# Kernel optimization log

Hardware: AMD Instinct MI355X
Metric: run time of the kernel (lower is better)

The kernel has to match this reference:

```python
import jax, jax.numpy as jnp
import numpy as np

L, B, S, D, H, FF = 6, 32, 512, 512, 8, 2048
DK = D // H
EPS = 1e-5
GELU_C = 0.7978845608028654  # sqrt(2/pi)
INV_SQRT_DK = 1.0 / float(np.sqrt(DK))


def gelu(x):
    return 0.5 * x * (1.0 + jnp.tanh(GELU_C * (x + 0.044715 * x ** 3)))


def layernorm(x, gamma, beta):
    m = jnp.mean(x, axis=-1, keepdims=True)
    v = jnp.mean(jnp.square(x - m), axis=-1, keepdims=True)
    return gamma * (x - m) / jnp.sqrt(v + EPS) + beta


def attention(x, WQ, WK, WV, WO):
    # NOTE: the original splits columns as (d_key, n_heads) on input,
    # and merges as (n_heads * d_key) on output -- replicated faithfully.
    q = (x @ WQ).reshape(B, S, DK, H).transpose(0, 3, 1, 2)  # (B,H,S,DK)
    k = (x @ WK).reshape(B, S, DK, H).transpose(0, 3, 2, 1)  # (B,H,DK,S)
    v = (x @ WV).reshape(B, S, DK, H).transpose(0, 3, 1, 2)  # (B,H,S,DK)
    score = jax.nn.softmax(jnp.matmul(q, k) * INV_SQRT_DK, axis=-1)  # (B,H,S,S)
    o = jnp.matmul(score, v).transpose(0, 2, 1, 3).reshape(B, S, H * DK)
    return o @ WO


def setup_inputs() -> dict:
    key = jax.random.key(0)
    ks = jax.random.split(key, 8)
    sc = 0.02
    return {
        "x": jax.random.normal(ks[0], (B, S, D), jnp.float32),
        "WQ": jax.random.normal(ks[1], (L, D, D), jnp.float32) * sc,
        "WK": jax.random.normal(ks[2], (L, D, D), jnp.float32) * sc,
        "WV": jax.random.normal(ks[3], (L, D, D), jnp.float32) * sc,
        "WO": jax.random.normal(ks[4], (L, D, D), jnp.float32) * sc,
        "K1": jax.random.normal(ks[5], (L, D, FF), jnp.float32) * sc,
        "B1": jnp.zeros((L, FF), jnp.float32),
        "K2": jax.random.normal(ks[6], (L, FF, D), jnp.float32) * sc,
        "B2": jnp.zeros((L, D), jnp.float32),
        "G1": jnp.ones((L, D), jnp.float32),
        "BE1": jnp.zeros((L, D), jnp.float32),
        "G2": jnp.ones((L, D), jnp.float32),
        "BE2": jnp.zeros((L, D), jnp.float32),
    }


def reference(x, WQ, WK, WV, WO, K1, B1, K2, B2, G1, BE1, G2, BE2):
    def step(h, p):
        wq, wk, wv, wo, k1, b1, k2, b2, g1, be1, g2, be2 = p
        h = layernorm(h + attention(h, wq, wk, wv, wo), g1, be1)
        f = gelu(h @ k1 + b1) @ k2 + b2
        h = layernorm(h + f, g2, be2)
        return h, None

    out, _ = jax.lax.scan(step, x, (WQ, WK, WV, WO, K1, B1, K2, B2, G1, BE1, G2, BE2))
    return out
```

## Files before the change

### kernel.cpp

```cpp
#include <hip/hip_runtime.h>
#include <hip/hip_bf16.h>
#include <stdint.h>

#define LB 6
#define BB 32
#define SS 512
#define DD 512
#define HH 8
#define FF_ 2048
#define MM (BB*SS)

typedef unsigned short u16;
typedef __attribute__((ext_vector_type(8))) short bf16x8;
typedef __attribute__((ext_vector_type(4))) float f32x4;

#define MFMA16(a,b,c) __builtin_amdgcn_mfma_f32_16x16x32_bf16((a),(b),(c),0,0,0)
#define GLD16(g, l) __builtin_amdgcn_global_load_lds( \
    (const __attribute__((address_space(1))) unsigned int*)(g), \
    (__attribute__((address_space(3))) unsigned int*)(l), 16, 0, 0)

__device__ __forceinline__ u16 f2b(float f){
  unsigned int u = __float_as_uint(f);
  u = u + 0x7FFFu + ((u >> 16) & 1u);
  return (u16)(u >> 16);
}

__device__ __forceinline__ float gelu_f(float x){
  float u = 0.7978845608028654f * (x + 0.044715f * x * x * x);
  return 0.5f * x * (1.0f + tanhf(u));
}

__global__ __launch_bounds__(256) void k_prep(const float* __restrict__ x,
                                              float* __restrict__ h,
                                              u16* __restrict__ hb){
  int i = blockIdx.x * 256 + threadIdx.x;
  float4 v = ((const float4*)x)[i];
  ((float4*)h)[i] = v;
  uint2 p;
  p.x = (unsigned)f2b(v.x) | ((unsigned)f2b(v.y) << 16);
  p.y = (unsigned)f2b(v.z) | ((unsigned)f2b(v.w) << 16);
  ((uint2*)hb)[i] = p;
}

__global__ __launch_bounds__(256) void k_wt(const float* __restrict__ in,
                                            u16* __restrict__ out, int K, int N){
  size_t ms = (size_t)K * N;
  in  += ms * blockIdx.z;
  out += ms * blockIdx.z;
  int n0 = blockIdx.x * 64, k0 = blockIdx.y * 64;
  __shared__ float tile[64][65];
  int t = threadIdx.x;
  int c = t & 63, rb = t >> 6;
  #pragma unroll
  for (int p = 0; p < 16; p++){
    int k = p * 4 + rb;
    tile[k][c] = in[(size_t)(k0 + k) * N + (n0 + c)];
  }
  __syncthreads();
  #pragma unroll
  for (int p = 0; p < 16; p++){
    int n = p * 4 + rb;
    out[(size_t)(n0 + n) * K + (k0 + c)] = f2b(tile[c][n]);
  }
}

template<int EPI, bool PERM>
__device__ __forceinline__ void gemm_body(const u16* __restrict__ A, const u16* __restrict__ Bt,
    const float* __restrict__ bias, float* __restrict__ outF, u16* __restrict__ outH,
    int N, int K)
{
  __shared__ u16 sA[128*32];
  __shared__ u16 sB[128*32];
  const int t = threadIdx.x;
  const int w = t >> 6, lane = t & 63, lr = lane & 15, lh = lane >> 4;
  const int bm = blockIdx.x * 128, bn = blockIdx.y * 128;
  const int wr = (w >> 1) * 64, wc = (w & 1) * 64;

  f32x4 acc[4][4];
  #pragma unroll
  for (int i = 0; i < 4; i++)
    #pragma unroll
    for (int j = 0; j < 4; j++) acc[i][j] = (f32x4){0.f,0.f,0.f,0.f};

  const int srow = t >> 2;
  const int scol = (t & 3) * 8;
  int b0 = bn + srow, b1 = bn + srow + 64;
  if (PERM){
    b0 = ((b0 & 63) << 3) | (b0 >> 6);
    b1 = ((b1 & 63) << 3) | (b1 >> 6);
  }
  const u16* gA0 = A  + (size_t)(bm + srow) * K + scol;
  const u16* gA1 = gA0 + (size_t)64 * K;
  const u16* gB0 = Bt + (size_t)b0 * K + scol;
  const u16* gB1 = Bt + (size_t)b1 * K + scol;
  u16* lA = sA + w * 512;
  u16* lB = sB + w * 512;

  for (int k0 = 0; k0 < K; k0 += 32){
    GLD16(gA0 + k0, lA);
    GLD16(gA1 + k0, lA + 2048);
    GLD16(gB0 + k0, lB);
    GLD16(gB1 + k0, lB + 2048);
    __syncthreads();
    bf16x8 af[4], bfr[4];
    #pragma unroll
    for (int i = 0; i < 4; i++) af[i]  = *(const bf16x8*)&sA[(wr + i*16 + lr)*32 + lh*8];
    #pragma unroll
    for (int j = 0; j < 4; j++) bfr[j] = *(const bf16x8*)&sB[(wc + j*16 + lr)*32 + lh*8];
    #pragma unroll
    for (int i = 0; i < 4; i++)
      #pragma unroll
      for (int j = 0; j < 4; j++)
        acc[i][j] = MFMA16(af[i], bfr[j], acc[i][j]);
    __syncthreads();
  }

  #pragma unroll
  for (int i = 0; i < 4; i++){
    int row = bm + wr + i*16 + lh*4;
    #pragma unroll
    for (int j = 0; j < 4; j++){
      int col = bn + wc + j*16 + lr;
      float bv = (EPI >= 2) ? bias[col] : 0.f;
      #pragma unroll
      for (int r = 0; r < 4; r++){
        float v = acc[i][j][r];
        size_t o = (size_t)(row + r) * N + col;
        if (EPI == 0) outH[o] = f2b(v);
        else if (EPI == 1) outF[o] = v;
        else if (EPI == 2) outH[o] = f2b(gelu_f(v + bv));
        else outF[o] = v + bv;
      }
    }
  }
}

template<int EPI>
__global__ __launch_bounds__(256) void k_gemm(const u16* A, const u16* Bt, const float* bias,
                                              float* outF, u16* outH, int N, int K){
  gemm_body<EPI,false>(A, Bt, bias, outF, outH, N, K);
}

__global__ __launch_bounds__(256) void k_qkv(const u16* A, const u16* Bq, const u16* Bk, const u16* Bv,
                                             u16* oq, u16* ok, u16* ov){
  const u16* Bt = (blockIdx.z == 0) ? Bq : (blockIdx.z == 1) ? Bk : Bv;
  u16* out = (blockIdx.z == 0) ? oq : (blockIdx.z == 1) ? ok : ov;
  gemm_body<0,true>(A, Bt, nullptr, nullptr, out, DD, DD);
}

__global__ __launch_bounds__(256) void k_attn(const u16* __restrict__ Q, const u16* __restrict__ Kp,
                                              const u16* __restrict__ V, u16* __restrict__ O){
  const int qt = blockIdx.x, hh = blockIdx.y, b = blockIdx.z;
  __shared__ u16 Qs[64*64];
  __shared__ u16 Ks[64*64];
  __shared__ u16 Vt[64*64];
  __shared__ u16 Ps[64*64];
  const int t = threadIdx.x, w = t >> 6, lane = t & 63, lr = lane & 15, lh = lane >> 4;
  const size_t base = ((size_t)b * SS) * DD + (size_t)hh * 64;

  const int srow = t >> 3;
  const int gcol = (((t & 7) ^ (srow & 7)) << 3);
  {
    const u16* g = Q + base + (size_t)(qt*64 + srow) * DD + gcol;
    GLD16(g,                   Qs + w*512);
    GLD16(g + (size_t)32*DD,   Qs + 2048 + w*512);
  }

  float mreg[4], lreg[4];
  f32x4 ofr[4];
  #pragma unroll
  for (int r = 0; r < 4; r++){ mreg[r] = -1e30f; lreg[r] = 0.f; }
  #pragma unroll
  for (int j = 0; j < 4; j++) ofr[j] = (f32x4){0.f,0.f,0.f,0.f};

  const int qswz = (lr & 7) << 3;

  for (int kt = 0; kt < 8; kt++){
    {
      const u16* g = Kp + base + (size_t)(kt*64 + srow) * DD + gcol;
      GLD16(g,                 Ks + w*512);
      GLD16(g + (size_t)32*DD, Ks + 2048 + w*512);
    }
    {
      const int dk0 = (t & 7) * 8, kv = (t >> 3) * 2;
      const u16* g = V + base + (size_t)(kt*64 + kv) * DD + dk0;
      uint4 r0 = *(const uint4*)g;
      uint4 r1 = *(const uint4*)(g + DD);
      const u16* e0 = (const u16*)&r0;
      const u16* e1 = (const u16*)&r1;
      #pragma unroll
      for (int i = 0; i < 8; i++){
        int dk = dk0 + i;
        int sw = ((((dk >> 3) ^ dk) & 7) << 3);
        *(unsigned int*)&Vt[dk*64 + (kv ^ sw)] =
            (unsigned int)e0[i] | ((unsigned int)e1[i] << 16);
      }
    }
    __syncthreads();

    bf16x8 a0 = *(const bf16x8*)&Qs[(w*16+lr)*64 + ((lh*8) ^ qswz)];
    bf16x8 a1 = *(const bf16x8*)&Qs[(w*16+lr)*64 + ((32 + lh*8) ^ qswz)];
    f32x4 sc[4];
    #pragma unroll
    for (int j = 0; j < 4; j++){
      bf16x8 b0 = *(const bf16x8*)&Ks[(j*16+lr)*64 + ((lh*8) ^ qswz)];
      bf16x8 b1 = *(const bf16x8*)&Ks[(j*16+lr)*64 + ((32 + lh*8) ^ qswz)];
      f32x4 z = (f32x4){0.f,0.f,0.f,0.f};
      z = MFMA16(a0, b0, z);
      z = MFMA16(a1, b1, z);
      sc[j] = z;
    }

    float pr[4][4];
    float esc[4];
    #pragma unroll
    for (int r = 0; r < 4; r++){
      float mx = fmaxf(fmaxf(sc[0][r], sc[1][r]), fmaxf(sc[2][r], sc[3][r]));
      mx = fmaxf(mx, __shfl_xor(mx, 1));
      mx = fmaxf(mx, __shfl_xor(mx, 2));
      mx = fmaxf(mx, __shfl_xor(mx, 4));
      mx = fmaxf(mx, __shfl_xor(mx, 8));
      mx *= 0.125f;
      float m2 = fmaxf(mreg[r], mx);
      float scl = __expf(mreg[r] - m2);
      mreg[r] = m2;
      float s = 0.f;
      #pragma unroll
      for (int j = 0; j < 4; j++){
        float p = __expf(sc[j][r]*0.125f - m2);
        pr[j][r] = p;
        s += p;
      }
      s += __shfl_xor(s, 1);
      s += __shfl_xor(s, 2);
      s += __shfl_xor(s, 4);
      s += __shfl_xor(s, 8);
      lreg[r] = lreg[r]*scl + s;
      esc[r] = scl;
    }

    #pragma unroll
    for (int j = 0; j < 4; j++)
      #pragma unroll
      for (int r = 0; r < 4; r++){
        int prow = w*16 + lh*4 + r;
        int pcol = j*16 + lr;
        Ps[prow*64 + (pcol ^ (((lh*4 + r) & 7) << 3))] = f2b(pr[j][r]);
      }

    #pragma unroll
    for (int j = 0; j < 4; j++)
      #pragma unroll
      for (int r = 0; r < 4; r++) ofr[j][r] *= esc[r];

    bf16x8 pa0 = *(const bf16x8*)&Ps[(w*16+lr)*64 + ((lh*8) ^ qswz)];
    bf16x8 pa1 = *(const bf16x8*)&Ps[(w*16+lr)*64 + ((32 + lh*8) ^ qswz)];
    #pragma unroll
    for (int j = 0; j < 4; j++){
      int dkr = j*16 + lr;
      int sw = ((((dkr >> 3) ^ dkr) & 7) << 3);
      bf16x8 v0 = *(const bf16x8*)&Vt[dkr*64 + ((lh*8) ^ sw)];
      bf16x8 v1 = *(const bf16x8*)&Vt[dkr*64 + ((32 + lh*8) ^ sw)];
      ofr[j] = MFMA16(pa0, v0, ofr[j]);
      ofr[j] = MFMA16(pa1, v1, ofr[j]);
    }
    __syncthreads();
  }

  #pragma unroll
  for (int j = 0; j < 4; j++)
    #pragma unroll
    for (int r = 0; r < 4; r++){
      float v = ofr[j][r] / lreg[r];
      O[base + (size_t)(qt*64 + w*16 + lh*4 + r) * DD + j*16 + lr] = f2b(v);
    }
}

__global__ __launch_bounds__(256) void k_ln(const float* __restrict__ hin, const float* __restrict__ add,
    const float* __restrict__ g, const float* __restrict__ be,
    float* __restrict__ hout, u16* __restrict__ hb){
  const int row = blockIdx.x;
  const int t = threadIdx.x;
  const size_t baseo = (size_t)row * DD;
  float v0 = hin[baseo + t]       + add[baseo + t];
  float v1 = hin[baseo + t + 256] + add[baseo + t + 256];
  float s = v0 + v1, q = v0*v0 + v1*v1;
  #pragma unroll
  for (int m = 32; m >= 1; m >>= 1){ s += __shfl_xor(s, m); q += __shfl_xor(q, m); }
  __shared__ float sh[8];
  const int w = t >> 6;
  if ((t & 63) == 0){ sh[w] = s; sh[4 + w] = q; }
  __syncthreads();
  s = sh[0] + sh[1] + sh[2] + sh[3];
  q = sh[4] + sh[5] + sh[6] + sh[7];
  float mean = s * (1.f/512.f);
  float var  = q * (1.f/512.f) - mean*mean;
  float rstd = rsqrtf(var + 1e-5f);
  float o0 = g[t]     * ((v0 - mean) * rstd) + be[t];
  float o1 = g[t+256] * ((v1 - mean) * rstd) + be[t+256];
  hout[baseo + t]       = o0;
  hout[baseo + t + 256] = o1;
  hb[baseo + t]       = f2b(o0);
  hb[baseo + t + 256] = f2b(o1);
}

extern "C" void kernel_launch(void* const* d_in, const int* in_sizes, int n_in,
                              void* d_out, int out_size, void* d_ws, size_t ws_size,
                              hipStream_t stream){
  const float* x   = (const float*)d_in[0];
  const float* WQ  = (const float*)d_in[1];
  const float* WK  = (const float*)d_in[2];
  const float* WV  = (const float*)d_in[3];
  const float* WO  = (const float*)d_in[4];
  const float* K1  = (const float*)d_in[5];
  const float* B1  = (const float*)d_in[6];
  const float* K2  = (const float*)d_in[7];
  const float* B2  = (const float*)d_in[8];
  const float* G1  = (const float*)d_in[9];
  const float* BE1 = (const float*)d_in[10];
  const float* G2  = (const float*)d_in[11];
  const float* BE2 = (const float*)d_in[12];
  float* hF = (float*)d_out;

  char* wp = (char*)d_ws;
  size_t off = 0;
  auto a16 = [&](size_t elems)->u16*{ u16* p = (u16*)(wp + off); off += elems*sizeof(u16); return p; };
  u16* WQt = a16((size_t)LB*DD*DD);
  u16* WKt = a16((size_t)LB*DD*DD);
  u16* WVt = a16((size_t)LB*DD*DD);
  u16* WOt = a16((size_t)LB*DD*DD);
  u16* K1t = a16((size_t)LB*DD*FF_);
  u16* K2t = a16((size_t)LB*DD*FF_);
  u16* hbf = a16((size_t)MM*DD);
  u16* qbf = a16((size_t)MM*DD);
  u16* kbf = a16((size_t)MM*DD);
  u16* vbf = a16((size_t)MM*DD);
  u16* abf = a16((size_t)MM*DD);
  u16* ff1 = qbf;
  float* tmpF = (float*)(wp + off); off += (size_t)MM*DD*sizeof(float);
  (void)ws_size; (void)in_sizes; (void)n_in; (void)out_size;

  k_prep<<<MM*DD/4/256, 256, 0, stream>>>(x, hF, hbf);
  k_wt<<<dim3(8,8,LB),        256, 0, stream>>>(WQ, WQt, DD, DD);
  k_wt<<<dim3(8,8,LB),        256, 0, stream>>>(WK, WKt, DD, DD);
  k_wt<<<dim3(8,8,LB),        256, 0, stream>>>(WV, WVt, DD, DD);
  k_wt<<<dim3(8,8,LB),        256, 0, stream>>>(WO, WOt, DD, DD);
  k_wt<<<dim3(FF_/64,8,LB),   256, 0, stream>>>(K1, K1t, DD, FF_);
  k_wt<<<dim3(8,FF_/64,LB),   256, 0, stream>>>(K2, K2t, FF_, DD);

  for (int l = 0; l < LB; l++){
    const u16* wq = WQt + (size_t)l*DD*DD;
    const u16* wk = WKt + (size_t)l*DD*DD;
    const u16* wv = WVt + (size_t)l*DD*DD;
    const u16* wo = WOt + (size_t)l*DD*DD;
    const u16* k1 = K1t + (size_t)l*DD*FF_;
    const u16* k2 = K2t + (size_t)l*DD*FF_;

    k_qkv<<<dim3(MM/128, DD/128, 3), 256, 0, stream>>>(hbf, wq, wk, wv, qbf, kbf, vbf);
    k_attn<<<dim3(SS/64, HH, BB), 256, 0, stream>>>(qbf, kbf, vbf, abf);
    k_gemm<1><<<dim3(MM/128, DD/128), 256, 0, stream>>>(abf, wo, nullptr, tmpF, nullptr, DD, DD);
    k_ln<<<MM, 256, 0, stream>>>(hF, tmpF, G1 + l*DD, BE1 + l*DD, hF, hbf);
    k_gemm<2><<<dim3(MM/128, FF_/128), 256, 0, stream>>>(hbf, k1, B1 + (size_t)l*FF_, nullptr, ff1, FF_, DD);
    k_gemm<3><<<dim3(MM/128, DD/128), 256, 0, stream>>>(ff1, k2, B2 + l*DD, tmpF, nullptr, DD, FF_);
    k_ln<<<MM, 256, 0, stream>>>(hF, tmpF, G2 + l*DD, BE2 + l*DD, hF, hbf);
  }
}
```

Baseline: 1.866 ms.

## Replace GEMMs with double-buffered 256-row 8-wave kernel, vectorize layernorm, cheaper GELU

```diff
diff --git a/kernel.cpp b/kernel.cpp
--- a/kernel.cpp
+++ b/kernel.cpp
@@ -18,6 +18,8 @@
 #define GLD16(g, l) __builtin_amdgcn_global_load_lds( \
     (const __attribute__((address_space(1))) unsigned int*)(g), \
     (__attribute__((address_space(3))) unsigned int*)(l), 16, 0, 0)
+#define BAR() asm volatile("s_barrier" ::: "memory")
+#define VMW(n) asm volatile("s_waitcnt vmcnt(" #n ")" ::: "memory")
 
 __device__ __forceinline__ u16 f2b(float f){
   unsigned int u = __float_as_uint(f);
@@ -26,8 +28,8 @@
 }
 
 __device__ __forceinline__ float gelu_f(float x){
-  float u = 0.7978845608028654f * (x + 0.044715f * x * x * x);
-  return 0.5f * x * (1.0f + tanhf(u));
+  float u2 = 1.5957691216057308f * (x + 0.044715f * x * x * x);
+  return x / (1.0f + __expf(-u2));
 }
 
 __global__ __launch_bounds__(256) void k_prep(const float* __restrict__ x,
@@ -64,68 +66,120 @@
   }
 }
 
-template<int EPI, bool PERM>
-__device__ __forceinline__ void gemm_body(const u16* __restrict__ A, const u16* __restrict__ Bt,
+template<int BN, int EPI, bool PERM>
+__global__ __launch_bounds__(512, 1) void k_gemm8(
+    const u16* __restrict__ A,
+    const u16* __restrict__ Bq, const u16* __restrict__ Bk, const u16* __restrict__ Bv,
     const float* __restrict__ bias, float* __restrict__ outF, u16* __restrict__ outH,
     int N, int K)
 {
-  __shared__ u16 sA[128*32];
-  __shared__ u16 sB[128*32];
+  constexpr int WM = (BN==256) ? 2 : 4;
+  constexpr int MR = 16/WM;
+  constexpr int MQ = MR/4;
+  constexpr int BHALF = (BN==256) ? 8192 : 4096;
+  constexpr int BBUF  = 2*BHALF;
+  constexpr int BL    = (BN==256) ? 2 : 1;
+  constexpr int HC    = (BN==256) ? 128 : 64;
+  __shared__ u16 sM[32768 + 2*BBUF];
+
   const int t = threadIdx.x;
-  const int w = t >> 6, lane = t & 63, lr = lane & 15, lh = lane >> 4;
-  const int bm = blockIdx.x * 128, bn = blockIdx.y * 128;
-  const int wr = (w >> 1) * 64, wc = (w & 1) * 64;
-
-  f32x4 acc[4][4];
-  #pragma unroll
-  for (int i = 0; i < 4; i++)
+  const int lane = t & 63, w = t >> 6, lr = lane & 15, lh = lane >> 4;
+  const int wm = (BN==256) ? (w>>2) : (w>>1);
+  const int wn = (BN==256) ? (w&3)  : (w&1);
+  const int bm = blockIdx.x * 256, bn = blockIdx.y * BN;
+  const int NTT = K >> 6, NIT = NTT >> 1;
+  const int tz = PERM ? (bn >> 9) : 0;
+
+  const int skA = (((t>>6)&1)<<5) + (((t>>4)&3)<<3);
+  const int srA = ((t>>7)<<4) + (t&15);
+  const u16* gA0 = A + (size_t)(bm +       srA) * K + skA;
+  const u16* gA1 = A + (size_t)(bm + 128 + srA) * K + skA;
+  const u16* gBp[2][2];
+  {
+    const u16* Bsel = PERM ? (tz==0 ? Bq : tz==1 ? Bk : Bv) : Bq;
+    #pragma unroll
+    for (int h = 0; h < 2; h++){
+      #pragma unroll
+      for (int s = 0; s < BL; s++){
+        int n = (PERM ? (bn & 511) : bn) + h*HC + srA + s*64;
+        int srow = PERM ? (((n & 63) << 3) | (n >> 6)) : n;
+        gBp[h][s] = Bsel + (size_t)srow * K + skA;
+      }
+    }
+  }
+
+  auto stageA = [&](int kt, int h){
+    u16* dst = sM + (kt&1)*16384 + h*8192 + t*8;
+    const u16* src = (h ? gA1 : gA0) + kt*64;
+    GLD16(src, dst);
+    GLD16(src + (size_t)64*K, dst + 4096);
+  };
+  auto stageB = [&](int kt, int h){
+    u16* dst = sM + 32768 + (kt&1)*BBUF + h*BHALF + t*8;
+    GLD16(gBp[h][0] + kt*64, dst);
+    if constexpr (BL == 2) GLD16(gBp[h][1] + kt*64, dst + 4096);
+  };
+
+  const int ha    = (BN==256) ? wm : (wm>>1);
+  const int mbase = (BN==256) ? 0  : ((wm&1)*4);
+  const int hbi   = (BN==256) ? (wn>>1) : wn;
+  const int nfb   = (BN==256) ? ((wn&1)*4) : 0;
+  const int rdAbase = ha*8192 + lane*8;
+  const int rdBbase = 32768 + hbi*BHALF + nfb*1024 + lane*8;
+
+  f32x4 acc[MR][4];
+  #pragma unroll
+  for (int i = 0; i < MR; i++)
     #pragma unroll
     for (int j = 0; j < 4; j++) acc[i][j] = (f32x4){0.f,0.f,0.f,0.f};
-
-  const int srow = t >> 2;
-  const int scol = (t & 3) * 8;
-  int b0 = bn + srow, b1 = bn + srow + 64;
-  if (PERM){
-    b0 = ((b0 & 63) << 3) | (b0 >> 6);
-    b1 = ((b1 & 63) << 3) | (b1 >> 6);
-  }
-  const u16* gA0 = A  + (size_t)(bm + srow) * K + scol;
-  const u16* gA1 = gA0 + (size_t)64 * K;
-  const u16* gB0 = Bt + (size_t)b0 * K + scol;
-  const u16* gB1 = Bt + (size_t)b1 * K + scol;
-  u16* lA = sA + w * 512;
-  u16* lB = sB + w * 512;
-
-  for (int k0 = 0; k0 < K; k0 += 32){
-    GLD16(gA0 + k0, lA);
-    GLD16(gA1 + k0, lA + 2048);
-    GLD16(gB0 + k0, lB);
-    GLD16(gB1 + k0, lB + 2048);
-    __syncthreads();
-    bf16x8 af[4], bfr[4];
-    #pragma unroll
-    for (int i = 0; i < 4; i++) af[i]  = *(const bf16x8*)&sA[(wr + i*16 + lr)*32 + lh*8];
-    #pragma unroll
-    for (int j = 0; j < 4; j++) bfr[j] = *(const bf16x8*)&sB[(wc + j*16 + lr)*32 + lh*8];
-    #pragma unroll
-    for (int i = 0; i < 4; i++)
-      #pragma unroll
-      for (int j = 0; j < 4; j++)
-        acc[i][j] = MFMA16(af[i], bfr[j], acc[i][j]);
-    __syncthreads();
-  }
-
-  #pragma unroll
-  for (int i = 0; i < 4; i++){
-    int row = bm + wr + i*16 + lh*4;
+  bf16x8 bfr[4][2];
+
+#define RD_A(d, q, af) { _Pragma("unroll") for (int i=0;i<MQ;i++){ _Pragma("unroll") for (int ks=0;ks<2;ks++) \
+    af[i][ks] = *(const bf16x8*)&sM[(d)*16384 + rdAbase + ((mbase + (q)*MQ + i)*2 + ks)*512]; } }
+#define RD_B(d) { _Pragma("unroll") for (int j=0;j<4;j++){ _Pragma("unroll") for (int ks=0;ks<2;ks++) \
+    bfr[j][ks] = *(const bf16x8*)&sM[(d)*BBUF + rdBbase + ((j)*2 + (ks))*512]; } }
+#define FMA_Q(q, af) { __builtin_amdgcn_s_setprio(1); \
+  _Pragma("unroll") for (int i=0;i<MQ;i++){ _Pragma("unroll") for (int j=0;j<4;j++){ _Pragma("unroll") for (int ks=0;ks<2;ks++) \
+    acc[(q)*MQ+i][j] = MFMA16(af[i][ks], bfr[j][ks], acc[(q)*MQ+i][j]); } } \
+  __builtin_amdgcn_s_setprio(0); }
+
+  stageA(0,0); stageA(0,1); stageB(0,0); stageB(0,1); stageB(1,0); stageB(1,1);
+  if constexpr (BL == 2) { VMW(4); } else { VMW(2); }
+  BAR();
+
+  for (int it = 0; it < NIT; ++it){
+    const int t0 = it*2;
+    const bool lastit = (it == NIT-1);
+    bf16x8 af[MQ][2];
+    RD_A(0,0,af); RD_B(0); stageA(t0+1, 0);            BAR(); FMA_Q(0, af); BAR();
+    RD_A(0,1,af);          stageA(t0+1, 1);            BAR(); FMA_Q(1, af); BAR();
+    RD_A(0,2,af); if (t0+2 < NTT) stageB(t0+2, 0);     BAR(); FMA_Q(2, af); BAR();
+    RD_A(0,3,af); if (t0+2 < NTT) stageB(t0+2, 1);     BAR(); FMA_Q(3, af);
+    if (lastit) { VMW(0); } else { if constexpr (BL == 2) { VMW(4); } else { VMW(2); } }
+    BAR();
+    RD_A(1,0,af); RD_B(1); if (t0+2 < NTT) stageA(t0+2, 0); BAR(); FMA_Q(0, af); BAR();
+    RD_A(1,1,af);          if (t0+2 < NTT) stageA(t0+2, 1); BAR(); FMA_Q(1, af); BAR();
+    RD_A(1,2,af); if (t0+3 < NTT) stageB(t0+3, 0);     BAR(); FMA_Q(2, af); BAR();
+    RD_A(1,3,af); if (t0+3 < NTT) stageB(t0+3, 1);     BAR(); FMA_Q(3, af);
+    if (!lastit) { if constexpr (BL == 2) { VMW(4); } else { VMW(2); } }
+    BAR();
+  }
+#undef RD_A
+#undef RD_B
+#undef FMA_Q
+
+  #pragma unroll
+  for (int mf = 0; mf < MR; mf++){
+    const int row = bm + wm*(256/WM) + mf*16 + lh*4;
     #pragma unroll
     for (int j = 0; j < 4; j++){
-      int col = bn + wc + j*16 + lr;
+      const int col = (PERM ? (bn & 511) : bn) + wn*64 + j*16 + lr;
       float bv = (EPI >= 2) ? bias[col] : 0.f;
       #pragma unroll
       for (int r = 0; r < 4; r++){
-        float v = acc[i][j][r];
+        float v = acc[mf][j][r];
         size_t o = (size_t)(row + r) * N + col;
+        if (PERM) o += (size_t)tz * ((size_t)MM * DD);
         if (EPI == 0) outH[o] = f2b(v);
         else if (EPI == 1) outF[o] = v;
         else if (EPI == 2) outH[o] = f2b(gelu_f(v + bv));
@@ -133,19 +187,6 @@
       }
     }
   }
-}
-
-template<int EPI>
-__global__ __launch_bounds__(256) void k_gemm(const u16* A, const u16* Bt, const float* bias,
-                                              float* outF, u16* outH, int N, int K){
-  gemm_body<EPI,false>(A, Bt, bias, outF, outH, N, K);
-}
-
-__global__ __launch_bounds__(256) void k_qkv(const u16* A, const u16* Bq, const u16* Bk, const u16* Bv,
-                                             u16* oq, u16* ok, u16* ov){
-  const u16* Bt = (blockIdx.z == 0) ? Bq : (blockIdx.z == 1) ? Bk : Bv;
-  u16* out = (blockIdx.z == 0) ? oq : (blockIdx.z == 1) ? ok : ov;
-  gemm_body<0,true>(A, Bt, nullptr, nullptr, out, DD, DD);
 }
 
 __global__ __launch_bounds__(256) void k_attn(const u16* __restrict__ Q, const u16* __restrict__ Kp,
@@ -279,29 +320,38 @@
 __global__ __launch_bounds__(256) void k_ln(const float* __restrict__ hin, const float* __restrict__ add,
     const float* __restrict__ g, const float* __restrict__ be,
     float* __restrict__ hout, u16* __restrict__ hb){
-  const int row = blockIdx.x;
-  const int t = threadIdx.x;
-  const size_t baseo = (size_t)row * DD;
-  float v0 = hin[baseo + t]       + add[baseo + t];
-  float v1 = hin[baseo + t + 256] + add[baseo + t + 256];
-  float s = v0 + v1, q = v0*v0 + v1*v1;
+  const int w = threadIdx.x >> 6, lane = threadIdx.x & 63;
+  const size_t row = (size_t)blockIdx.x * 4 + w;
+  const size_t base = row * DD + lane * 8;
+  float4 xa = *(const float4*)&hin[base];
+  float4 xb = *(const float4*)&hin[base + 4];
+  float4 aa = *(const float4*)&add[base];
+  float4 ab = *(const float4*)&add[base + 4];
+  float v[8] = { xa.x+aa.x, xa.y+aa.y, xa.z+aa.z, xa.w+aa.w,
+                 xb.x+ab.x, xb.y+ab.y, xb.z+ab.z, xb.w+ab.w };
+  float s = 0.f, q = 0.f;
+  #pragma unroll
+  for (int e = 0; e < 8; e++){ s += v[e]; q += v[e]*v[e]; }
   #pragma unroll
   for (int m = 32; m >= 1; m >>= 1){ s += __shfl_xor(s, m); q += __shfl_xor(q, m); }
-  __shared__ float sh[8];
-  const int w = t >> 6;
-  if ((t & 63) == 0){ sh[w] = s; sh[4 + w] = q; }
-  __syncthreads();
-  s = sh[0] + sh[1] + sh[2] + sh[3];
-  q = sh[4] + sh[5] + sh[6] + sh[7];
   float mean = s * (1.f/512.f);
   float var  = q * (1.f/512.f) - mean*mean;
   float rstd = rsqrtf(var + 1e-5f);
-  float o0 = g[t]     * ((v0 - mean) * rstd) + be[t];
-  float o1 = g[t+256] * ((v1 - mean) * rstd) + be[t+256];
-  hout[baseo + t]       = o0;
-  hout[baseo + t + 256] = o1;
-  hb[baseo + t]       = f2b(o0);
-  hb[baseo + t + 256] = f2b(o1);
+  float4 g0 = *(const float4*)&g[lane*8],  g1 = *(const float4*)&g[lane*8+4];
+  float4 b0 = *(const float4*)&be[lane*8], b1 = *(const float4*)&be[lane*8+4];
+  float gv[8] = {g0.x,g0.y,g0.z,g0.w,g1.x,g1.y,g1.z,g1.w};
+  float bv[8] = {b0.x,b0.y,b0.z,b0.w,b1.x,b1.y,b1.z,b1.w};
+  float o[8];
+  #pragma unroll
+  for (int e = 0; e < 8; e++) o[e] = gv[e] * ((v[e]-mean)*rstd) + bv[e];
+  *(float4*)&hout[base]     = make_float4(o[0],o[1],o[2],o[3]);
+  *(float4*)&hout[base + 4] = make_float4(o[4],o[5],o[6],o[7]);
+  uint4 pk;
+  pk.x = (unsigned)f2b(o[0]) | ((unsigned)f2b(o[1])<<16);
+  pk.y = (unsigned)f2b(o[2]) | ((unsigned)f2b(o[3])<<16);
+  pk.z = (unsigned)f2b(o[4]) | ((unsigned)f2b(o[5])<<16);
+  pk.w = (unsigned)f2b(o[6]) | ((unsigned)f2b(o[7])<<16);
+  *(uint4*)&hb[base] = pk;
 }
 
 extern "C" void kernel_launch(void* const* d_in, const int* in_sizes, int n_in,
@@ -356,12 +406,12 @@
     const u16* k1 = K1t + (size_t)l*DD*FF_;
     const u16* k2 = K2t + (size_t)l*DD*FF_;
 
-    k_qkv<<<dim3(MM/128, DD/128, 3), 256, 0, stream>>>(hbf, wq, wk, wv, qbf, kbf, vbf);
+    k_gemm8<256,0,true ><<<dim3(64,6), 512, 0, stream>>>(hbf, wq, wk, wv, nullptr, nullptr, qbf, DD, DD);
     k_attn<<<dim3(SS/64, HH, BB), 256, 0, stream>>>(qbf, kbf, vbf, abf);
-    k_gemm<1><<<dim3(MM/128, DD/128), 256, 0, stream>>>(abf, wo, nullptr, tmpF, nullptr, DD, DD);
-    k_ln<<<MM, 256, 0, stream>>>(hF, tmpF, G1 + l*DD, BE1 + l*DD, hF, hbf);
-    k_gemm<2><<<dim3(MM/128, FF_/128), 256, 0, stream>>>(hbf, k1, B1 + (size_t)l*FF_, nullptr, ff1, FF_, DD);
-    k_gemm<3><<<dim3(MM/128, DD/128), 256, 0, stream>>>(ff1, k2, B2 + l*DD, tmpF, nullptr, DD, FF_);
-    k_ln<<<MM, 256, 0, stream>>>(hF, tmpF, G2 + l*DD, BE2 + l*DD, hF, hbf);
-  }
-}
+    k_gemm8<128,1,false><<<dim3(64,4), 512, 0, stream>>>(abf, wo, wo, wo, nullptr, tmpF, nullptr, DD, DD);
+    k_ln<<<MM/4, 256, 0, stream>>>(hF, tmpF, G1 + l*DD, BE1 + l*DD, hF, hbf);
+    k_gemm8<256,2,false><<<dim3(64,8), 512, 0, stream>>>(hbf, k1, k1, k1, B1 + (size_t)l*FF_, nullptr, ff1, FF_, DD);
+    k_gemm8<128,3,false><<<dim3(64,4), 512, 0, stream>>>(ff1, k2, k2, k2, B2 + l*DD, tmpF, nullptr, DD, FF_);
+    k_ln<<<MM/4, 256, 0, stream>>>(hF, tmpF, G2 + l*DD, BE2 + l*DD, hF, hbf);
+  }
+}
```

After: 1.854 ms. About the same (-0.7%).
